# Kernel tuning notes

Hardware: AMD Instinct MI355X
Metric: run time of the kernel (lower is better)

The kernel has to match this reference:

```python
import jax, jax.numpy as jnp
import numpy as np

D_MODEL = 1024
NUM_HEADS = 16
D_K = D_MODEL // NUM_HEADS
THETA = 10000.0
BATCH, SEQ = 2, 2048


def apply_rope(x, token_positions, theta):
    # x: [..., heads, seq, d_k]; interleaved pair rotation
    d = x.shape[-1]
    inv_freq = theta ** (-jnp.arange(0, d, 2, dtype=jnp.float32) / d)  # [d/2]
    ang = token_positions.astype(jnp.float32)[:, None] * inv_freq[None, :]  # [seq, d/2]
    cos, sin = jnp.cos(ang), jnp.sin(ang)  # broadcast over batch/heads
    x_even = x[..., 0::2]
    x_odd = x[..., 1::2]
    out_even = x_even * cos - x_odd * sin
    out_odd = x_even * sin + x_odd * cos
    out = jnp.stack([out_even, out_odd], axis=-1)  # [..., seq, d/2, 2]
    return out.reshape(x.shape)


def setup_inputs() -> dict:
    key = jax.random.key(0)
    ks = jax.random.split(key, 5)
    scale = 1.0 / np.sqrt(D_MODEL)
    return {
        "x": jax.random.normal(ks[0], (BATCH, SEQ, D_MODEL), dtype=jnp.float32),
        "wq": jax.random.normal(ks[1], (D_MODEL, D_MODEL), dtype=jnp.float32) * scale,
        "wk": jax.random.normal(ks[2], (D_MODEL, D_MODEL), dtype=jnp.float32) * scale,
        "wv": jax.random.normal(ks[3], (D_MODEL, D_MODEL), dtype=jnp.float32) * scale,
        "wo": jax.random.normal(ks[4], (D_MODEL, D_MODEL), dtype=jnp.float32) * scale,
        "token_positions": jnp.arange(SEQ, dtype=jnp.int32),
    }


def reference(x, wq, wk, wv, wo, token_positions):
    B, S, _ = x.shape
    # fused-style QKV projections: weight layout is [d_out, d_in]
    xq = jnp.einsum("bsd,kd->bsk", x, wq)
    xk = jnp.einsum("bsd,kd->bsk", x, wk)
    xv = jnp.einsum("bsd,vd->bsv", x, wv)
    # split heads: [b, h, s, d_h]
    def split(t):
        return t.reshape(B, S, NUM_HEADS, D_K).transpose(0, 2, 1, 3)
    xq, xk, xv = split(xq), split(xk), split(xv)
    xq = apply_rope(xq, token_positions, THETA)
    xk = apply_rope(xk, token_positions, THETA)
    scores = jnp.einsum("bhqd,bhkd->bhqk", xq, xk) / jnp.sqrt(jnp.float32(D_K))
    causal = jnp.tril(jnp.ones((S, S), dtype=bool))
    scores = jnp.where(causal, scores, -jnp.inf)
    attn = jax.nn.softmax(scores, axis=-1)
    out = jnp.einsum("bhqk,bhkd->bhqd", attn, xv)
    out = out.transpose(0, 2, 1, 3).reshape(B, S, D_MODEL)  # merge heads
    return jnp.einsum("bsv,dv->bsd", out, wo)
```

## Files before the change

kernel.cpp:

```cpp
#include <hip/hip_runtime.h>

typedef __attribute__((ext_vector_type(8))) short short8;
typedef __attribute__((ext_vector_type(4))) short short4v;
typedef __attribute__((ext_vector_type(4))) float floatx4;

__device__ inline float b2f(ushort u) {
    union { uint i; float f; } c; c.i = ((uint)u) << 16; return c.f;
}
__device__ inline ushort f2b(float f) {
    union { uint i; float f; } c; c.f = f;
    uint i = c.i;
    uint r = (i + 0x7FFFu + ((i >> 16) & 1u)) >> 16;
    return (ushort)r;
}
__device__ inline ushort f2b_fast(float f) {
    union { uint i; float f; } c; c.f = f;
    return (ushort)((c.i + 0x8000u) >> 16);
}

__device__ __forceinline__ void load_lds16(const ushort* g, ushort* l) {
    __builtin_amdgcn_global_load_lds((const __attribute__((address_space(1))) void*)g,
                                     (__attribute__((address_space(3))) void*)l, 16, 0, 0);
}

__global__ __launch_bounds__(256) void rope_tab_k(const int* __restrict__ pos,
                                                  float2* __restrict__ tab) {
    const int idx = blockIdx.x * 256 + threadIdx.x;
    const int s = idx >> 5, fi = idx & 31;
    const float inv = exp2f(-(float)fi * 0.41524101186092557f);
    const float ang = (float)pos[s] * inv;
    float sn, cs;
    sincosf(ang, &sn, &cs);
    tab[idx] = make_float2(cs, sn);
}

__global__ __launch_bounds__(256) void cvt4_k(const float* __restrict__ x,
                                              const float* __restrict__ wq,
                                              const float* __restrict__ wk,
                                              const float* __restrict__ wv,
                                              ushort* __restrict__ xb,
                                              ushort* __restrict__ wqb,
                                              ushort* __restrict__ wkb,
                                              ushort* __restrict__ wvb) {
    const int blk = blockIdx.x;
    const float* in; ushort* out; int base;
    if (blk < 2048)      { in = x;  out = xb;  base = blk; }
    else if (blk < 2560) { in = wq; out = wqb; base = blk - 2048; }
    else if (blk < 3072) { in = wk; out = wkb; base = blk - 2560; }
    else                 { in = wv; out = wvb; base = blk - 3072; }
    const int i = (base * 256 + threadIdx.x) * 8;
    float4 f0 = *(const float4*)(in + i);
    float4 f1 = *(const float4*)(in + i + 4);
    ushort u[8] = {f2b(f0.x), f2b(f0.y), f2b(f0.z), f2b(f0.w),
                   f2b(f1.x), f2b(f1.y), f2b(f1.z), f2b(f1.w)};
    *(uint4*)(out + i) = *(const uint4*)u;
}

__global__ __launch_bounds__(256) void cvt_k(const float* __restrict__ in,
                                             ushort* __restrict__ out, int n) {
    const int i = (blockIdx.x * 256 + threadIdx.x) * 8;
    if (i >= n) return;
    float4 f0 = *(const float4*)(in + i);
    float4 f1 = *(const float4*)(in + i + 4);
    ushort u[8] = {f2b(f0.x), f2b(f0.y), f2b(f0.z), f2b(f0.w),
                   f2b(f1.x), f2b(f1.y), f2b(f1.z), f2b(f1.w)};
    *(uint4*)(out + i) = *(const uint4*)u;
}

template <bool OUTF32>
__device__ __forceinline__ void gemm_body(ushort* As, ushort* Bs,
                                          const ushort* __restrict__ A,
                                          const ushort* __restrict__ B,
                                          void* __restrict__ C,
                                          int N, int m0, int n0,
                                          bool doRope, const float2* __restrict__ tab) {
    const int tid = threadIdx.x;
    const int wave = tid >> 6, lane = tid & 63;
    const int quad = lane >> 4, l16 = lane & 15;
    const int wm = (wave >> 1) * 64, wn = (wave & 1) * 64;

    floatx4 acc[4][4] = {};

    const ushort* ga[4];
    const ushort* gb[4];
    int lofs[4];
#pragma unroll
    for (int m = 0; m < 4; ++m) {
        const int c = tid + m * 256;
        const int row = c >> 3;
        const int jg = (c & 7) ^ (row & 7);
        lofs[m] = c * 8;
        ga[m] = A + (size_t)(m0 + row) * 1024 + jg * 8;
        gb[m] = B + (size_t)(n0 + row) * 1024 + jg * 8;
    }

    for (int kt = 0; kt < 16; ++kt) {
        __syncthreads();
#pragma unroll
        for (int m = 0; m < 4; ++m) {
            load_lds16(ga[m] + kt * 64, As + lofs[m]);
            load_lds16(gb[m] + kt * 64, Bs + lofs[m]);
        }
        __syncthreads();
#pragma unroll
        for (int half = 0; half < 2; ++half) {
            short8 af[4], bf[4];
            const int j = half * 4 + quad;
#pragma unroll
            for (int i = 0; i < 4; ++i) {
                const int ra = wm + i * 16 + l16;
                const int rb = wn + i * 16 + l16;
                af[i] = *(const short8*)(As + ra * 64 + (j ^ (ra & 7)) * 8);
                bf[i] = *(const short8*)(Bs + rb * 64 + (j ^ (rb & 7)) * 8);
            }
#pragma unroll
            for (int mi = 0; mi < 4; ++mi)
#pragma unroll
                for (int ni = 0; ni < 4; ++ni)
                    acc[mi][ni] = __builtin_amdgcn_mfma_f32_16x16x32_bf16(af[mi], bf[ni], acc[mi][ni], 0, 0, 0);
        }
    }
#pragma unroll
    for (int mi = 0; mi < 4; ++mi) {
        const int row = m0 + wm + mi * 16 + quad * 4;
#pragma unroll
        for (int ni = 0; ni < 4; ++ni) {
            const int col = n0 + wn + ni * 16 + l16;
            const int fi = ((wn + ni * 16 + l16) & 63) >> 1;
#pragma unroll
            for (int r = 0; r < 4; ++r) {
                float v = acc[mi][ni][r];
                if (doRope) {
                    const float other = __shfl_xor(v, 1);
                    const float2 cs = tab[((row + r) & 2047) * 32 + fi];
                    v = (col & 1) ? (other * cs.y + v * cs.x) : (v * cs.x - other * cs.y);
                }
                if (OUTF32) ((float*)C)[(size_t)(row + r) * N + col] = v;
                else        ((ushort*)C)[(size_t)(row + r) * N + col] = f2b(v);
            }
        }
    }
}

__global__ __launch_bounds__(256) void gemm_qkv(const ushort* __restrict__ xb,
                                                const ushort* __restrict__ wqb,
                                                const ushort* __restrict__ wkb,
                                                const ushort* __restrict__ wvb,
                                                ushort* __restrict__ q,
                                                ushort* __restrict__ k,
                                                ushort* __restrict__ vt,
                                                const float2* __restrict__ tab) {
    __shared__ __align__(16) ushort As[8192], Bs[8192];
    const int blk = blockIdx.x;
    const int job = blk >> 8, r = blk & 255;
    const ushort *A, *B;
    ushort* C;
    int N, m0, n0;
    bool rope;
    if (job == 0)      { A = xb;  B = wqb; C = q;  N = 1024; m0 = (r >> 3) * 128; n0 = (r & 7) * 128; rope = true; }
    else if (job == 1) { A = xb;  B = wkb; C = k;  N = 1024; m0 = (r >> 3) * 128; n0 = (r & 7) * 128; rope = true; }
    else               { A = wvb; B = xb;  C = vt; N = 4096; m0 = (r & 7) * 128;  n0 = (r >> 3) * 128; rope = false; }
    gemm_body<false>(As, Bs, A, B, C, N, m0, n0, rope, tab);
}

__global__ __launch_bounds__(256) void gemm_o(const ushort* __restrict__ A,
                                              const ushort* __restrict__ B,
                                              float* __restrict__ C) {
    __shared__ __align__(16) ushort As[8192], Bs[8192];
    gemm_body<true>(As, Bs, A, B, C, 1024, blockIdx.y * 128, blockIdx.x * 128, false, nullptr);
}

__global__ __launch_bounds__(256) void attn_k(const ushort* __restrict__ Qg,
                                              const ushort* __restrict__ Kg,
                                              const ushort* __restrict__ Vtg,
                                              ushort* __restrict__ Og) {
    __shared__ __align__(16) ushort Ks[2][4096];
    __shared__ __align__(16) ushort Vs[2][4096];

    const int tid = threadIdx.x;
    const int wave = tid >> 6, lane = tid & 63;
    const int quad = lane >> 4, l16 = lane & 15;
    const int blk = blockIdx.x;
    const int bh = blk & 31, pr = blk >> 5;
    const int b = bh >> 4, h = bh & 15;
    const int bq = b * 2048;
    const int wl = wave * 16 + l16;

    const int cA = tid, cB = tid + 256;
    const int sA = cA >> 3, jA = ((cA & 7) - sA) & 7;
    const int sB = cB >> 3, jB = ((cB & 7) - sB) & 7;
    const ushort* kgA = Kg + (size_t)(bq + sA) * 1024 + h * 64 + jA * 8;
    const ushort* kgB = Kg + (size_t)(bq + sB) * 1024 + h * 64 + jB * 8;
    const ushort* vgA = Vtg + (size_t)(h * 64 + sA) * 4096 + bq + jA * 8;
    const ushort* vgB = Vtg + (size_t)(h * 64 + sB) * 4096 + bq + jB * 8;

    const float SCL = 0.18033688011112042f;

    for (int half = 0; half < 2; ++half) {
        const int qt = half ? (31 - pr) : pr;
        const int nk = qt + 1;
        const int dt = nk - 1;

        const ushort* qrow = Qg + (size_t)(bq + qt * 64 + wl) * 1024 + h * 64 + quad * 8;
        const short8 qf0 = *(const short8*)qrow;
        const short8 qf1 = *(const short8*)(qrow + 32);

        floatx4 od[4] = {};
        float l_st = 0.0f;

        load_lds16(kgA, &Ks[0][cA * 8]);
        load_lds16(kgB, &Ks[0][cB * 8]);
        load_lds16(vgA, &Vs[0][cA * 8]);
        load_lds16(vgB, &Vs[0][cB * 8]);
        __syncthreads();

        for (int kt = 0; kt < nk; ++kt) {
            const int cur = kt & 1;
            if (kt + 1 < nk) {
                const int nxt = cur ^ 1;
                load_lds16(kgA + (size_t)(kt + 1) * 65536, &Ks[nxt][cA * 8]);
                load_lds16(kgB + (size_t)(kt + 1) * 65536, &Ks[nxt][cB * 8]);
                load_lds16(vgA + (kt + 1) * 64, &Vs[nxt][cA * 8]);
                load_lds16(vgB + (kt + 1) * 64, &Vs[nxt][cB * 8]);
            }
            const ushort* kb = Ks[cur];
            const ushort* vb = Vs[cur];

            floatx4 st[4];
#pragma unroll
            for (int cb = 0; cb < 4; ++cb) {
                const int s = cb * 16 + l16;
                const int ch0 = s * 8 + ((quad + s) & 7);
                const int ch1 = s * 8 + ((quad + 4 + s) & 7);
                short8 kf0 = *(const short8*)(kb + ch0 * 8);
                short8 kf1 = *(const short8*)(kb + ch1 * 8);
                floatx4 z = {};
                z = __builtin_amdgcn_mfma_f32_16x16x32_bf16(kf0, qf0, z, 0, 0, 0);
                z = __builtin_amdgcn_mfma_f32_16x16x32_bf16(kf1, qf1, z, 0, 0, 0);
                st[cb] = z;
            }

            const bool diag = (kt == dt);
            float pv[4][4];
            float sum = 0.0f;
#pragma unroll
            for (int cb = 0; cb < 4; ++cb) {
                const int scb = cb * 16 + quad * 4;
#pragma unroll
                for (int r = 0; r < 4; ++r) {
                    float e = exp2f(st[cb][r] * SCL);
                    if (diag && (scb + r > wl)) e = 0.0f;
                    pv[cb][r] = e;
                    sum += e;
                }
            }
            sum += __shfl_xor(sum, 16);
            sum += __shfl_xor(sum, 32);
            l_st += sum;

            short4v pb[4];
#pragma unroll
            for (int cb = 0; cb < 4; ++cb) {
                short4v pk;
#pragma unroll
                for (int r = 0; r < 4; ++r) pk[r] = (short)f2b_fast(pv[cb][r]);
                pb[cb] = pk;
            }
#pragma unroll
            for (int db = 0; db < 4; ++db) {
                const int d = db * 16 + l16;
#pragma unroll
                for (int cb = 0; cb < 4; ++cb) {
                    const int j = cb * 2 + (quad >> 1);
                    const int ch = d * 8 + ((j + d) & 7);
                    short4v vf = *(const short4v*)(vb + ch * 8 + (quad & 1) * 4);
                    od[db] = __builtin_amdgcn_mfma_f32_16x16x16bf16_1k(vf, pb[cb], od[db], 0, 0, 0);
                }
            }
            __syncthreads();
        }

        const float linv = 1.0f / l_st;
        ushort* orow = Og + (size_t)(bq + qt * 64 + wl) * 1024 + h * 64 + quad * 4;
#pragma unroll
        for (int db = 0; db < 4; ++db) {
            uint2 w;
            w.x = (uint)f2b(od[db][0] * linv) | ((uint)f2b(od[db][1] * linv) << 16);
            w.y = (uint)f2b(od[db][2] * linv) | ((uint)f2b(od[db][3] * linv) << 16);
            *(uint2*)(orow + db * 16) = w;
        }
    }
}

extern "C" void kernel_launch(void* const* d_in, const int* in_sizes, int n_in,
                              void* d_out, int out_size, void* d_ws, size_t ws_size,
                              hipStream_t stream) {
    const float* x  = (const float*)d_in[0];
    const float* wq = (const float*)d_in[1];
    const float* wk = (const float*)d_in[2];
    const float* wv = (const float*)d_in[3];
    const float* wo = (const float*)d_in[4];
    const int* pos  = (const int*)d_in[5];

    const size_t NX = (size_t)4096 * 1024;
    const size_t NW = (size_t)1024 * 1024;

    ushort* q_ws  = (ushort*)d_ws;
    ushort* k_ws  = q_ws + NX;
    ushort* vt_ws = k_ws + NX;
    ushort* o_ws  = vt_ws + NX;
    ushort* xb  = (ushort*)d_out;
    ushort* wqb = xb + NX;
    ushort* wkb = wqb + NW;
    ushort* wvb = wkb + NW;
    float2* tab = (float2*)(wvb + NW);

    rope_tab_k<<<dim3(256), 256, 0, stream>>>(pos, tab);
    cvt4_k<<<dim3(3584), 256, 0, stream>>>(x, wq, wk, wv, xb, wqb, wkb, wvb);
    gemm_qkv<<<dim3(768), 256, 0, stream>>>(xb, wqb, wkb, wvb, q_ws, k_ws, vt_ws, tab);
    attn_k<<<dim3(512), 256, 0, stream>>>(q_ws, k_ws, vt_ws, o_ws);
    cvt_k<<<dim3(512), 256, 0, stream>>>(wo, q_ws, (int)NW);
    gemm_o<<<dim3(8, 32), 256, 0, stream>>>(o_ws, q_ws, (float*)d_out);
}
```

Before: 214.7 us.

## Double-buffer GEMM LDS tiles with K=32 stages to overlap loads and MFMA

The GEMM main loop moves from a single-buffered K=64 tile with two barriers per step to a double-buffered K=32 tile. The next tile's global-to-LDS load is issued before the MFMAs on the current buffer, and there is one barrier per iteration. The LDS swizzle changes from an XOR over 8 chunks to a rotation over 4 chunks to match the narrower rows. This hides global load latency behind compute, at the cost of twice as many iterations, so more barriers in total. It also relies on the LDS allocations being large enough to hold two 4096-element buffers.

```diff
diff --git a/kernel.cpp b/kernel.cpp
--- a/kernel.cpp
+++ b/kernel.cpp
@@ -81,44 +81,45 @@
 
     floatx4 acc[4][4] = {};
 
-    const ushort* ga[4];
-    const ushort* gb[4];
-    int lofs[4];
-#pragma unroll
-    for (int m = 0; m < 4; ++m) {
-        const int c = tid + m * 256;
-        const int row = c >> 3;
-        const int jg = (c & 7) ^ (row & 7);
-        lofs[m] = c * 8;
-        ga[m] = A + (size_t)(m0 + row) * 1024 + jg * 8;
-        gb[m] = B + (size_t)(n0 + row) * 1024 + jg * 8;
-    }
-
-    for (int kt = 0; kt < 16; ++kt) {
+    const int cA = tid, cB = tid + 256;
+    const int rA = cA >> 2, jgA = ((cA & 3) - (rA >> 1)) & 3;
+    const int rB = cB >> 2, jgB = ((cB & 3) - (rB >> 1)) & 3;
+    const ushort* gaA = A + (size_t)(m0 + rA) * 1024 + jgA * 8;
+    const ushort* gaB = A + (size_t)(m0 + rB) * 1024 + jgB * 8;
+    const ushort* gbA = B + (size_t)(n0 + rA) * 1024 + jgA * 8;
+    const ushort* gbB = B + (size_t)(n0 + rB) * 1024 + jgB * 8;
+
+    load_lds16(gaA, As + cA * 8);
+    load_lds16(gaB, As + cB * 8);
+    load_lds16(gbA, Bs + cA * 8);
+    load_lds16(gbB, Bs + cB * 8);
+    __syncthreads();
+
+    for (int kt = 0; kt < 32; ++kt) {
+        const int cur = kt & 1;
+        if (kt + 1 < 32) {
+            const int nb = (cur ^ 1) * 4096;
+            load_lds16(gaA + (kt + 1) * 32, As + nb + cA * 8);
+            load_lds16(gaB + (kt + 1) * 32, As + nb + cB * 8);
+            load_lds16(gbA + (kt + 1) * 32, Bs + nb + cA * 8);
+            load_lds16(gbB + (kt + 1) * 32, Bs + nb + cB * 8);
+        }
+        const ushort* as = As + cur * 4096;
+        const ushort* bs = Bs + cur * 4096;
+        short8 af[4], bf[4];
+#pragma unroll
+        for (int i = 0; i < 4; ++i) {
+            const int ra = wm + i * 16 + l16;
+            const int rb = wn + i * 16 + l16;
+            af[i] = *(const short8*)(as + ra * 32 + (((quad + (ra >> 1)) & 3) << 3));
+            bf[i] = *(const short8*)(bs + rb * 32 + (((quad + (rb >> 1)) & 3) << 3));
+        }
+#pragma unroll
+        for (int mi = 0; mi < 4; ++mi)
+#pragma unroll
+            for (int ni = 0; ni < 4; ++ni)
+                acc[mi][ni] = __builtin_amdgcn_mfma_f32_16x16x32_bf16(af[mi], bf[ni], acc[mi][ni], 0, 0, 0);
         __syncthreads();
-#pragma unroll
-        for (int m = 0; m < 4; ++m) {
-            load_lds16(ga[m] + kt * 64, As + lofs[m]);
-            load_lds16(gb[m] + kt * 64, Bs + lofs[m]);
-        }
-        __syncthreads();
-#pragma unroll
-        for (int half = 0; half < 2; ++half) {
-            short8 af[4], bf[4];
-            const int j = half * 4 + quad;
-#pragma unroll
-            for (int i = 0; i < 4; ++i) {
-                const int ra = wm + i * 16 + l16;
-                const int rb = wn + i * 16 + l16;
-                af[i] = *(const short8*)(As + ra * 64 + (j ^ (ra & 7)) * 8);
-                bf[i] = *(const short8*)(Bs + rb * 64 + (j ^ (rb & 7)) * 8);
-            }
-#pragma unroll
-            for (int mi = 0; mi < 4; ++mi)
-#pragma unroll
-                for (int ni = 0; ni < 4; ++ni)
-                    acc[mi][ni] = __builtin_amdgcn_mfma_f32_16x16x32_bf16(af[mi], bf[ni], acc[mi][ni], 0, 0, 0);
-        }
     }
 #pragma unroll
     for (int mi = 0; mi < 4; ++mi) {
```

Result: faster. 204.4 us (-4.8%).
